# Optimization experiments

Hardware: AMD Instinct MI355X
Metric: run time of the kernel (lower is better)

Reference implementation:

```python
import jax, jax.numpy as jnp
import numpy as np
from jax import lax

EMBED = 512
HEADS = 8
KD = EMBED // HEADS  # key_dim == head_dim (value_factor=1)


def setup_inputs() -> dict:
    key = jax.random.key(0)
    ks = jax.random.split(key, 13)
    b, h, w = 4, 128, 128
    s = 0.02
    return {
        "x": jax.random.normal(ks[0], (b, h, w, EMBED), jnp.float32),
        "mask_h": jax.random.normal(ks[1], (HEADS, h, h), jnp.float32),
        "mask_w": jax.random.normal(ks[2], (HEADS, w, w), jnp.float32),
        "Wq": jax.random.normal(ks[3], (EMBED, EMBED), jnp.float32) * s,
        "bq": jnp.zeros((EMBED,), jnp.float32),
        "Wk": jax.random.normal(ks[4], (EMBED, EMBED), jnp.float32) * s,
        "bk": jnp.zeros((EMBED,), jnp.float32),
        "Wv": jax.random.normal(ks[5], (EMBED, EMBED), jnp.float32) * s,
        "bv": jnp.zeros((EMBED,), jnp.float32),
        "lepe_w": jax.random.normal(ks[6], (5, 5, 1, EMBED), jnp.float32) * s,  # depthwise 5x5, HWIO
        "lepe_b": jnp.zeros((EMBED,), jnp.float32),
        "Wo": jax.random.normal(ks[7], (EMBED, EMBED), jnp.float32) * s,
        "bo": jnp.zeros((EMBED,), jnp.float32),
    }


def reference(x, mask_h, mask_w, Wq, bq, Wk, bk, Wv, bv, lepe_w, lepe_b, Wo, bo):
    b, h, w, _ = x.shape
    scaling = KD ** -0.5
    q = x @ Wq + bq                      # (b,h,w,C)
    k = (x @ Wk + bk) * scaling
    v = x @ Wv + bv

    # depthwise-conv positional term (LePE), 5x5 pad 2, groups=C
    lepe = lax.conv_general_dilated(
        v, lepe_w, window_strides=(1, 1), padding=[(2, 2), (2, 2)],
        dimension_numbers=("NHWC", "HWIO", "NHWC"), feature_group_count=EMBED,
    ) + lepe_b

    qr = q.reshape(b, h, w, HEADS, KD)
    kr = k.reshape(b, h, w, HEADS, KD)
    vr = v.reshape(b, h, w, HEADS, KD)

    # width-axis attention (per row), additive per-head decay mask
    sw = jnp.einsum("bhqnd,bhknd->bhnqk", qr, kr) + mask_w[None, None]  # (b,h,n,w,w)
    Aw = jax.nn.softmax(sw, axis=-1)
    o1 = jnp.einsum("bhnqk,bhknd->bhqnd", Aw, vr)                       # (b,h,w,n,d)

    # height-axis attention (per column) on the width-pass output
    sh = jnp.einsum("bqwnd,bkwnd->bwnqk", qr, kr) + mask_h[None, None]  # (b,w,n,h,h)
    Ah = jax.nn.softmax(sh, axis=-1)
    o2 = jnp.einsum("bwnqk,bkwnd->bqwnd", Ah, o1)                       # (b,h,w,n,d)

    out = o2.reshape(b, h, w, EMBED) + lepe
    return out @ Wo + bo
```

## Files before the change

kernel.cpp:

```cpp
#include <hip/hip_runtime.h>
#include <stdint.h>
#include <stddef.h>

typedef unsigned short u16;
typedef __attribute__((ext_vector_type(8))) short bf16x8;
typedef __attribute__((ext_vector_type(4))) float f32x4;

__device__ __forceinline__ u16 f2bf(float f) {
  union { float f; uint32_t u; } v; v.f = f;
  uint32_t u = v.u;
  return (u16)((u + 0x7FFFu + ((u >> 16) & 1u)) >> 16);
}
__device__ __forceinline__ float bf2f(u16 b) {
  union { uint32_t u; float f; } v; v.u = ((uint32_t)b) << 16;
  return v.f;
}

__device__ __forceinline__ void glds16(const u16* g, u16* l) {
  __builtin_amdgcn_global_load_lds((const __attribute__((address_space(1))) void*)g,
                                   (__attribute__((address_space(3))) void*)l, 16, 0, 0);
}

#define MFMA(a, b, c) __builtin_amdgcn_mfma_f32_16x16x32_bf16((a), (b), (c), 0, 0, 0)


__global__ __launch_bounds__(256) void k_cvt_bf16(const float* __restrict__ in,
                                                  u16* __restrict__ out, int n) {
  int i = (blockIdx.x * 256 + threadIdx.x) * 8;
  if (i >= n) return;
  const float4* p = (const float4*)(in + i);
  float4 a = p[0], b = p[1];
  union { bf16x8 v; u16 s[8]; } o;
  o.s[0] = f2bf(a.x); o.s[1] = f2bf(a.y); o.s[2] = f2bf(a.z); o.s[3] = f2bf(a.w);
  o.s[4] = f2bf(b.x); o.s[5] = f2bf(b.y); o.s[6] = f2bf(b.z); o.s[7] = f2bf(b.w);
  *(bf16x8*)(out + i) = o.v;
}

__global__ __launch_bounds__(256) void k_build_wqkv(
    const float* __restrict__ Wq, const float* __restrict__ bq,
    const float* __restrict__ Wk, const float* __restrict__ bk,
    const float* __restrict__ Wv, const float* __restrict__ bv,
    u16* __restrict__ wT, float* __restrict__ bias) {
  int idx = blockIdx.x * 256 + threadIdx.x;
  int n = idx >> 9, k = idx & 511;
  const float* W; const float* B; int nn; float s = 1.0f;
  if (n < 512)       { W = Wq; B = bq; nn = n; }
  else if (n < 1024) { W = Wk; B = bk; nn = n - 512; s = 0.125f; }
  else               { W = Wv; B = bv; nn = n - 1024; }
  wT[idx] = f2bf(W[(size_t)k * 512 + nn] * s);
  if (k == 0) bias[n] = B[nn] * s;
}

__global__ __launch_bounds__(256) void k_build_wo(const float* __restrict__ Wo,
                                                  u16* __restrict__ wT) {
  int idx = blockIdx.x * 256 + threadIdx.x;
  int n = idx >> 9, k = idx & 511;
  wT[idx] = f2bf(Wo[(size_t)k * 512 + n]);
}


__device__ __forceinline__ void stageH(const u16* __restrict__ src, int ld, size_t grow0,
                                       int kt, int row0, u16* lmat, int t) {
  #pragma unroll
  for (int it = 0; it < 2; ++it) {
    int e = it * 4096 + t * 8;
    int row = row0 + (e >> 6);
    int ch = (e >> 3) & 7;
    int cs = ch ^ (row & 7);
    glds16(src + (grow0 + row) * (size_t)ld + kt * 64 + cs * 8, lmat + row * 64 + ch * 8);
  }
}

__device__ __forceinline__ bf16x8 ldfrag(const u16* lmat, int row, int c) {
  return *(const bf16x8*)(lmat + row * 64 + ((c ^ (row & 7)) << 3));
}

template<bool STAGE, bool VM8>
__device__ __forceinline__ void process_tile(
    const u16* __restrict__ A, int lda, size_t rowA0,
    const u16* __restrict__ BT, int ldb, size_t rowB0,
    u16* LAc, u16* LBc, int nxt,
    int wm, int wn, int fq, int fr, int t,
    f32x4 (&acc)[2][4][2][2])
{
  bf16x8 bA[4][2], bB[2][2][2];
  #pragma unroll
  for (int n = 0; n < 2; ++n)
    #pragma unroll
    for (int kk = 0; kk < 2; ++kk)
      bB[0][n][kk] = ldfrag(LBc, wn * 32 + n * 16 + fr, kk * 4 + fq);
  #pragma unroll
  for (int m = 0; m < 4; ++m)
    #pragma unroll
    for (int kk = 0; kk < 2; ++kk)
      bA[m][kk] = ldfrag(LAc, wm * 64 + m * 16 + fr, kk * 4 + fq);
  __builtin_amdgcn_s_setprio(1);
  #pragma unroll
  for (int m = 0; m < 4; ++m)
    #pragma unroll
    for (int n = 0; n < 2; ++n)
      #pragma unroll
      for (int kk = 0; kk < 2; ++kk)
        acc[0][m][0][n] = MFMA(bA[m][kk], bB[0][n][kk], acc[0][m][0][n]);
  __builtin_amdgcn_s_setprio(0);
  __builtin_amdgcn_s_barrier();
  #pragma unroll
  for (int n = 0; n < 2; ++n)
    #pragma unroll
    for (int kk = 0; kk < 2; ++kk)
      bB[1][n][kk] = ldfrag(LBc, 128 + wn * 32 + n * 16 + fr, kk * 4 + fq);
  if (STAGE) {
    stageH(A, lda, rowA0, nxt, 0, LAc, t);
    stageH(BT, ldb, rowB0, nxt, 0, LBc, t);
  }
  __builtin_amdgcn_s_setprio(1);
  #pragma unroll
  for (int m = 0; m < 4; ++m)
    #pragma unroll
    for (int n = 0; n < 2; ++n)
      #pragma unroll
      for (int kk = 0; kk < 2; ++kk)
        acc[0][m][1][n] = MFMA(bA[m][kk], bB[1][n][kk], acc[0][m][1][n]);
  __builtin_amdgcn_s_setprio(0);
  __builtin_amdgcn_s_barrier();
  #pragma unroll
  for (int m = 0; m < 4; ++m)
    #pragma unroll
    for (int kk = 0; kk < 2; ++kk)
      bA[m][kk] = ldfrag(LAc, 128 + wm * 64 + m * 16 + fr, kk * 4 + fq);
  if (STAGE) stageH(BT, ldb, rowB0, nxt, 128, LBc, t);
  __builtin_amdgcn_s_setprio(1);
  #pragma unroll
  for (int m = 0; m < 4; ++m)
    #pragma unroll
    for (int n = 0; n < 2; ++n)
      #pragma unroll
      for (int kk = 0; kk < 2; ++kk)
        acc[1][m][0][n] = MFMA(bA[m][kk], bB[0][n][kk], acc[1][m][0][n]);
  __builtin_amdgcn_s_setprio(0);
  __builtin_amdgcn_s_barrier();
  if (STAGE) stageH(A, lda, rowA0, nxt, 128, LAc, t);
  __builtin_amdgcn_s_setprio(1);
  #pragma unroll
  for (int m = 0; m < 4; ++m)
    #pragma unroll
    for (int n = 0; n < 2; ++n)
      #pragma unroll
      for (int kk = 0; kk < 2; ++kk)
        acc[1][m][1][n] = MFMA(bA[m][kk], bB[1][n][kk], acc[1][m][1][n]);
  __builtin_amdgcn_s_setprio(0);
  if (VM8) asm volatile("s_waitcnt vmcnt(8)" ::: "memory");
  else     asm volatile("s_waitcnt vmcnt(0)" ::: "memory");
  __builtin_amdgcn_s_barrier();
}

template<bool OUT_F32, int NTN>
__global__ __launch_bounds__(512, 2) void k_gemm256(
    const u16* __restrict__ A, int lda,
    const u16* __restrict__ BT, int ldb,
    const float* __restrict__ bias,
    void* __restrict__ Cp, int ldc)
{
  __shared__ u16 lds[65536];
  u16* LA0 = lds;
  u16* LB0 = lds + 16384;
  u16* LA1 = lds + 32768;
  u16* LB1 = lds + 49152;

  const int t = threadIdx.x, l = t & 63, w = t >> 6;
  const int wm = w >> 2, wn = w & 3;
  const int fq = l >> 4, fr = l & 15;

  const int bid = blockIdx.x;
  const int cpx = gridDim.x >> 3;
  const int swz = (bid & 7) * cpx + (bid >> 3);
  const int tn = swz % NTN, tm = swz / NTN;
  const size_t rowA0 = (size_t)tm * 256;
  const size_t rowB0 = (size_t)tn * 256;

  f32x4 acc[2][4][2][2];
  #pragma unroll
  for (int a = 0; a < 2; ++a)
    #pragma unroll
    for (int m = 0; m < 4; ++m)
      #pragma unroll
      for (int b = 0; b < 2; ++b)
        #pragma unroll
        for (int n = 0; n < 2; ++n) acc[a][m][b][n] = (f32x4){0.f, 0.f, 0.f, 0.f};

  stageH(A,  lda, rowA0, 0, 0,   LA0, t); stageH(A,  lda, rowA0, 0, 128, LA0, t);
  stageH(BT, ldb, rowB0, 0, 0,   LB0, t); stageH(BT, ldb, rowB0, 0, 128, LB0, t);
  stageH(A,  lda, rowA0, 1, 0,   LA1, t); stageH(A,  lda, rowA0, 1, 128, LA1, t);
  stageH(BT, ldb, rowB0, 1, 0,   LB1, t); stageH(BT, ldb, rowB0, 1, 128, LB1, t);
  asm volatile("s_waitcnt vmcnt(8)" ::: "memory");
  __builtin_amdgcn_s_barrier();

  for (int i = 0; i < 3; ++i) {
    process_tile<true, true>(A, lda, rowA0, BT, ldb, rowB0, LA0, LB0, 2 * i + 2,
                             wm, wn, fq, fr, t, acc);
    process_tile<true, true>(A, lda, rowA0, BT, ldb, rowB0, LA1, LB1, 2 * i + 3,
                             wm, wn, fq, fr, t, acc);
  }
  process_tile<false, false>(A, lda, rowA0, BT, ldb, rowB0, LA0, LB0, 0,
                             wm, wn, fq, fr, t, acc);
  process_tile<false, false>(A, lda, rowA0, BT, ldb, rowB0, LA1, LB1, 0,
                             wm, wn, fq, fr, t, acc);

  #pragma unroll
  for (int nh = 0; nh < 2; ++nh)
    #pragma unroll
    for (int n = 0; n < 2; ++n) {
      int col = (int)rowB0 + nh * 128 + wn * 32 + n * 16 + fr;
      float bb = bias[col];
      #pragma unroll
      for (int mh = 0; mh < 2; ++mh)
        #pragma unroll
        for (int m = 0; m < 4; ++m) {
          #pragma unroll
          for (int r = 0; r < 4; ++r) {
            size_t row = rowA0 + mh * 128 + wm * 64 + m * 16 + fq * 4 + r;
            float v = acc[mh][m][nh][n][r] + bb;
            if (OUT_F32) ((float*)Cp)[row * ldc + col] = v;
            else         ((u16*)Cp)[row * ldc + col] = f2bf(v);
          }
        }
    }
}


__global__ __launch_bounds__(256) void k_lepe(
    const u16* __restrict__ qkv, const float* __restrict__ w5,
    const float* __restrict__ lb, u16* __restrict__ outp)
{
  __shared__ u16 wlds[12800];
  #pragma unroll
  for (int j = 0; j < 50; ++j) {
    int idx = j * 256 + threadIdx.x;
    wlds[idx] = f2bf(w5[idx]);
  }
  __syncthreads();

  const int t = threadIdx.x, w = t >> 6, l = t & 63;
  const int c0 = l << 3;
  const int bid = blockIdx.x;
  const int x = (bid & 31) * 4 + w;
  const int y0 = ((bid >> 5) & 15) * 8;
  const int b = bid >> 9;

  float acc[8][8];
  {
    float4 b0 = *(const float4*)(lb + c0);
    float4 b1 = *(const float4*)(lb + c0 + 4);
    #pragma unroll
    for (int tt = 0; tt < 8; ++tt) {
      acc[tt][0] = b0.x; acc[tt][1] = b0.y; acc[tt][2] = b0.z; acc[tt][3] = b0.w;
      acc[tt][4] = b1.x; acc[tt][5] = b1.y; acc[tt][6] = b1.z; acc[tt][7] = b1.w;
    }
  }

  #pragma unroll
  for (int r = 0; r < 12; ++r) {
    int yy = y0 + r - 2;
    if ((unsigned)yy < 128u) {
      #pragma unroll
      for (int dx = 0; dx < 5; ++dx) {
        int xx = x + dx - 2;
        if ((unsigned)xx < 128u) {
          union { bf16x8 v; u16 s[8]; } v8;
          v8.v = *(const bf16x8*)(qkv + (size_t)((b * 128 + yy) * 128 + xx) * 1536
                                  + 1024 + c0);
          float vf[8];
          #pragma unroll
          for (int j = 0; j < 8; ++j) vf[j] = bf2f(v8.s[j]);
          #pragma unroll
          for (int tt = 0; tt < 8; ++tt) {
            int dy = r - tt;
            if (dy >= 0 && dy <= 4) {
              union { bf16x8 v; u16 s[8]; } w8;
              w8.v = *(const bf16x8*)(wlds + (dy * 5 + dx) * 512 + c0);
              #pragma unroll
              for (int j = 0; j < 8; ++j)
                acc[tt][j] += vf[j] * bf2f(w8.s[j]);
            }
          }
        }
      }
    }
  }

  #pragma unroll
  for (int tt = 0; tt < 8; ++tt) {
    size_t tok = (size_t)(b * 128 + y0 + tt) * 128 + x;
    union { bf16x8 v; u16 s[8]; } ov;
    #pragma unroll
    for (int j = 0; j < 8; ++j) ov.s[j] = f2bf(acc[tt][j]);
    *(bf16x8*)(outp + tok * 512 + c0) = ov.v;
  }
}


template<int AXIS>
__global__ __launch_bounds__(256) void k_attn(
    const u16* qkv, const float* __restrict__ mask,
    const u16* __restrict__ lepe, u16* outp)
{
  __shared__ u16 smem[24576];
  u16* q_s = smem;
  u16* k_s = smem + 8192;
  u16* vT  = smem + 16384;
  u16* P   = smem;

  const int t = threadIdx.x, w = t >> 6, l = t & 63;
  const int line = blockIdx.x, head = blockIdx.y, b = blockIdx.z;
  const int coff = head * 64;
  const size_t base0 = (AXIS == 0) ? ((size_t)(b * 128 + line) * 128)
                                   : ((size_t)b * 16384 + line);
  const size_t tstr = (AXIS == 0) ? 1 : 128;

  const int e0 = w * 512 + l * 8;
  #pragma unroll
  for (int it = 0; it < 4; ++it) {
    int ee = it * 2048 + e0;
    int row = ee >> 6;
    int cs = ((ee >> 3) & 7) ^ (row & 7);
    size_t tok = base0 + (size_t)row * tstr;
    glds16(qkv + tok * 1536 +       coff + cs * 8, q_s + it * 2048 + w * 512);
    glds16(qkv + tok * 1536 + 512 + coff + cs * 8, k_s + it * 2048 + w * 512);
  }
  {
    int kl = ((t >> 7) << 4) + (t & 15);
    int chunk = (t >> 4) & 7;
    #pragma unroll
    for (int p = 0; p < 4; ++p) {
      int kidx = p * 32 + kl;
      size_t tok = base0 + (size_t)kidx * tstr;
      union { bf16x8 v; u16 s[8]; } v8;
      v8.v = *(const bf16x8*)(qkv + tok * 1536 + 1024 + coff + chunk * 8);
      #pragma unroll
      for (int j = 0; j < 8; ++j) {
        int d = chunk * 8 + j;
        int byt = d * 256 + ((2 * kidx) ^ (j << 4));
        *(u16*)((char*)vT + byt) = v8.s[j];
      }
    }
  }
  __syncthreads();

  f32x4 acc[2][8];
  #pragma unroll
  for (int m = 0; m < 2; ++m)
    #pragma unroll
    for (int n = 0; n < 8; ++n) acc[m][n] = (f32x4){0.f, 0.f, 0.f, 0.f};

  #pragma unroll
  for (int kk = 0; kk < 2; ++kk) {
    bf16x8 af[2];
    #pragma unroll
    for (int m = 0; m < 2; ++m) {
      int row = w * 32 + m * 16 + (l & 15);
      int c = (kk * 4 + (l >> 4)) ^ (row & 7);
      af[m] = *(const bf16x8*)(q_s + row * 64 + c * 8);
    }
    #pragma unroll
    for (int n = 0; n < 8; ++n) {
      int row = n * 16 + (l & 15);
      int c = (kk * 4 + (l >> 4)) ^ (row & 7);
      bf16x8 bfr = *(const bf16x8*)(k_s + row * 64 + c * 8);
      acc[0][n] = MFMA(af[0], bfr, acc[0][n]);
      acc[1][n] = MFMA(af[1], bfr, acc[1][n]);
    }
  }

  const float* mbase = mask + (size_t)head * 16384;
  #pragma unroll
  for (int m = 0; m < 2; ++m) {
    int q0 = w * 32 + m * 16 + ((l >> 4) << 2);
    #pragma unroll
    for (int n = 0; n < 8; ++n) {
      const float* mp = mbase + (size_t)q0 * 128 + n * 16 + (l & 15);
      #pragma unroll
      for (int r = 0; r < 4; ++r) acc[m][n][r] += mp[(size_t)r * 128];
    }
    #pragma unroll
    for (int r = 0; r < 4; ++r) {
      float mx = acc[m][0][r];
      #pragma unroll
      for (int n = 1; n < 8; ++n) mx = fmaxf(mx, acc[m][n][r]);
      mx = fmaxf(mx, __shfl_xor(mx, 1));
      mx = fmaxf(mx, __shfl_xor(mx, 2));
      mx = fmaxf(mx, __shfl_xor(mx, 4));
      mx = fmaxf(mx, __shfl_xor(mx, 8));
      float sum = 0.f;
      #pragma unroll
      for (int n = 0; n < 8; ++n) {
        float ev = __expf(acc[m][n][r] - mx);
        acc[m][n][r] = ev; sum += ev;
      }
      sum += __shfl_xor(sum, 1);
      sum += __shfl_xor(sum, 2);
      sum += __shfl_xor(sum, 4);
      sum += __shfl_xor(sum, 8);
      float inv = 1.0f / sum;
      #pragma unroll
      for (int n = 0; n < 8; ++n) acc[m][n][r] *= inv;
    }
  }
  __syncthreads();

  #pragma unroll
  for (int m = 0; m < 2; ++m) {
    #pragma unroll
    for (int r = 0; r < 4; ++r) {
      int row = w * 32 + m * 16 + ((l >> 4) << 2) + r;
      int swz = (row & 7) << 4;
      #pragma unroll
      for (int n = 0; n < 8; ++n) {
        int col = n * 16 + (l & 15);
        *(u16*)((char*)P + row * 256 + ((2 * col) ^ swz)) = f2bf(acc[m][n][r]);
      }
    }
  }
  __syncthreads();

  f32x4 o[2][4];
  #pragma unroll
  for (int m = 0; m < 2; ++m)
    #pragma unroll
    for (int n = 0; n < 4; ++n) o[m][n] = (f32x4){0.f, 0.f, 0.f, 0.f};

  #pragma unroll
  for (int kt = 0; kt < 4; ++kt) {
    bf16x8 af[2];
    #pragma unroll
    for (int m = 0; m < 2; ++m) {
      int row = w * 32 + m * 16 + (l & 15);
      af[m] = *(const bf16x8*)((const char*)P + row * 256 +
               ((((kt * 4 + (l >> 4)) << 4)) ^ ((row & 7) << 4)));
    }
    #pragma unroll
    for (int n = 0; n < 4; ++n) {
      int d = n * 16 + (l & 15);
      int byt = d * 256 + (((kt * 32 + (l >> 4) * 8) * 2) ^ ((d & 7) << 4));
      bf16x8 bfr = *(const bf16x8*)((const char*)vT + byt);
      o[0][n] = MFMA(af[0], bfr, o[0][n]);
      o[1][n] = MFMA(af[1], bfr, o[1][n]);
    }
  }

  #pragma unroll
  for (int m = 0; m < 2; ++m) {
    #pragma unroll
    for (int r = 0; r < 4; ++r) {
      int i = w * 32 + m * 16 + ((l >> 4) << 2) + r;
      size_t tok = base0 + (size_t)i * tstr;
      #pragma unroll
      for (int n = 0; n < 4; ++n) {
        int d = n * 16 + (l & 15);
        float v = o[m][n][r];
        if (AXIS == 1) {
          v += bf2f(lepe[tok * 512 + coff + d]);
          outp[tok * 1536 + coff + d] = f2bf(v);
        } else {
          outp[tok * 1536 + 1024 + coff + d] = f2bf(v);
        }
      }
    }
  }
}


extern "C" void kernel_launch(void* const* d_in, const int* in_sizes, int n_in,
                              void* d_out, int out_size, void* d_ws, size_t ws_size,
                              hipStream_t stream) {
  const float* x  = (const float*)d_in[0];
  const float* mh = (const float*)d_in[1];
  const float* mw = (const float*)d_in[2];
  const float* Wq = (const float*)d_in[3];
  const float* bq = (const float*)d_in[4];
  const float* Wk = (const float*)d_in[5];
  const float* bk = (const float*)d_in[6];
  const float* Wv = (const float*)d_in[7];
  const float* bv = (const float*)d_in[8];
  const float* w5 = (const float*)d_in[9];
  const float* lb = (const float*)d_in[10];
  const float* Wo = (const float*)d_in[11];
  const float* bo = (const float*)d_in[12];

  char* ws = (char*)d_ws;
  u16*   qkv   = (u16*)ws;
  u16*   wqkvT = (u16*)(ws + 201326592);
  u16*   woT   = (u16*)(ws + 202899456);
  float* bqkv  = (float*)(ws + 203423744);

  char* od = (char*)d_out;
  u16* xb   = (u16*)od;
  u16* lepe = (u16*)(od + 67108864);

  k_cvt_bf16<<<16384, 256, 0, stream>>>(x, xb, 33554432);
  k_build_wqkv<<<3072, 256, 0, stream>>>(Wq, bq, Wk, bk, Wv, bv, wqkvT, bqkv);
  k_build_wo<<<1024, 256, 0, stream>>>(Wo, woT);

  k_gemm256<false, 6><<<1536, 512, 0, stream>>>(xb, 512, wqkvT, 512, bqkv, qkv, 1536);

  k_lepe<<<2048, 256, 0, stream>>>(qkv, w5, lb, lepe);

  k_attn<0><<<dim3(128, 8, 4), 256, 0, stream>>>(qkv, mw, nullptr, qkv);
  k_attn<1><<<dim3(128, 8, 4), 256, 0, stream>>>(qkv, mh, lepe, qkv);

  k_gemm256<true, 2><<<512, 512, 0, stream>>>(qkv, 1536, woT, 512, bo, d_out, 512);
}
```

Before: 456.7 us.

## Prefetch next K-tile LDS fragments during last MFMA quadrant of GEMM

Restructures the 256x256 GEMM main loop so the A/B register fragments for the next K tile are read from the other LDS buffer during the final MFMA quadrant of the current tile, with fragments carried across calls in persistent register arrays. It adds explicit lgkmcnt(0) waits before barriers, casts LDS reads to address-space-3 pointers, and stops unrolling the outer loop. The aim is to hide LDS read latency behind MFMA work, at the cost of more live registers and extra waits.

Measured after the change: 762.3 us. +66.9%, slower.

```diff
diff --git a/kernel.cpp b/kernel.cpp
--- a/kernel.cpp
+++ b/kernel.cpp
@@ -5,6 +5,8 @@
 typedef unsigned short u16;
 typedef __attribute__((ext_vector_type(8))) short bf16x8;
 typedef __attribute__((ext_vector_type(4))) float f32x4;
+
+typedef __attribute__((address_space(3))) const bf16x8* lds_frag_cptr;
 
 __device__ __forceinline__ u16 f2bf(float f) {
   union { float f; uint32_t u; } v; v.f = f;
@@ -72,43 +74,28 @@
 }
 
 __device__ __forceinline__ bf16x8 ldfrag(const u16* lmat, int row, int c) {
-  return *(const bf16x8*)(lmat + row * 64 + ((c ^ (row & 7)) << 3));
-}
-
-template<bool STAGE, bool VM8>
+  const u16* p = lmat + row * 64 + ((c ^ (row & 7)) << 3);
+  return *(lds_frag_cptr)p;
+}
+
+#define LGKM0_BAR() do { \
+    asm volatile("s_waitcnt lgkmcnt(0)" ::: "memory"); \
+    __builtin_amdgcn_s_barrier(); } while (0)
+
+template<bool STAGE, bool NEXTRD, int VMN>
 __device__ __forceinline__ void process_tile(
     const u16* __restrict__ A, int lda, size_t rowA0,
     const u16* __restrict__ BT, int ldb, size_t rowB0,
-    u16* LAc, u16* LBc, int nxt,
+    u16* LAc, u16* LBc, u16* LAo, u16* LBo, int nxt,
     int wm, int wn, int fq, int fr, int t,
+    bf16x8 (&fA)[2][4][2], bf16x8 (&fB)[2][2][2],
     f32x4 (&acc)[2][4][2][2])
 {
-  bf16x8 bA[4][2], bB[2][2][2];
   #pragma unroll
   for (int n = 0; n < 2; ++n)
     #pragma unroll
     for (int kk = 0; kk < 2; ++kk)
-      bB[0][n][kk] = ldfrag(LBc, wn * 32 + n * 16 + fr, kk * 4 + fq);
-  #pragma unroll
-  for (int m = 0; m < 4; ++m)
-    #pragma unroll
-    for (int kk = 0; kk < 2; ++kk)
-      bA[m][kk] = ldfrag(LAc, wm * 64 + m * 16 + fr, kk * 4 + fq);
-  __builtin_amdgcn_s_setprio(1);
-  #pragma unroll
-  for (int m = 0; m < 4; ++m)
-    #pragma unroll
-    for (int n = 0; n < 2; ++n)
-      #pragma unroll
-      for (int kk = 0; kk < 2; ++kk)
-        acc[0][m][0][n] = MFMA(bA[m][kk], bB[0][n][kk], acc[0][m][0][n]);
-  __builtin_amdgcn_s_setprio(0);
-  __builtin_amdgcn_s_barrier();
-  #pragma unroll
-  for (int n = 0; n < 2; ++n)
-    #pragma unroll
-    for (int kk = 0; kk < 2; ++kk)
-      bB[1][n][kk] = ldfrag(LBc, 128 + wn * 32 + n * 16 + fr, kk * 4 + fq);
+      fB[1][n][kk] = ldfrag(LBc, 128 + wn * 32 + n * 16 + fr, kk * 4 + fq);
   if (STAGE) {
     stageH(A, lda, rowA0, nxt, 0, LAc, t);
     stageH(BT, ldb, rowB0, nxt, 0, LBc, t);
@@ -120,14 +107,14 @@
     for (int n = 0; n < 2; ++n)
       #pragma unroll
       for (int kk = 0; kk < 2; ++kk)
-        acc[0][m][1][n] = MFMA(bA[m][kk], bB[1][n][kk], acc[0][m][1][n]);
+        acc[0][m][0][n] = MFMA(fA[0][m][kk], fB[0][n][kk], acc[0][m][0][n]);
   __builtin_amdgcn_s_setprio(0);
-  __builtin_amdgcn_s_barrier();
+  LGKM0_BAR();
   #pragma unroll
   for (int m = 0; m < 4; ++m)
     #pragma unroll
     for (int kk = 0; kk < 2; ++kk)
-      bA[m][kk] = ldfrag(LAc, 128 + wm * 64 + m * 16 + fr, kk * 4 + fq);
+      fA[1][m][kk] = ldfrag(LAc, 128 + wm * 64 + m * 16 + fr, kk * 4 + fq);
   if (STAGE) stageH(BT, ldb, rowB0, nxt, 128, LBc, t);
   __builtin_amdgcn_s_setprio(1);
   #pragma unroll
@@ -136,9 +123,9 @@
     for (int n = 0; n < 2; ++n)
       #pragma unroll
       for (int kk = 0; kk < 2; ++kk)
-        acc[1][m][0][n] = MFMA(bA[m][kk], bB[0][n][kk], acc[1][m][0][n]);
+        acc[0][m][1][n] = MFMA(fA[0][m][kk], fB[1][n][kk], acc[0][m][1][n]);
   __builtin_amdgcn_s_setprio(0);
-  __builtin_amdgcn_s_barrier();
+  LGKM0_BAR();
   if (STAGE) stageH(A, lda, rowA0, nxt, 128, LAc, t);
   __builtin_amdgcn_s_setprio(1);
   #pragma unroll
@@ -147,11 +134,33 @@
     for (int n = 0; n < 2; ++n)
       #pragma unroll
       for (int kk = 0; kk < 2; ++kk)
-        acc[1][m][1][n] = MFMA(bA[m][kk], bB[1][n][kk], acc[1][m][1][n]);
+        acc[1][m][0][n] = MFMA(fA[1][m][kk], fB[0][n][kk], acc[1][m][0][n]);
   __builtin_amdgcn_s_setprio(0);
-  if (VM8) asm volatile("s_waitcnt vmcnt(8)" ::: "memory");
-  else     asm volatile("s_waitcnt vmcnt(0)" ::: "memory");
-  __builtin_amdgcn_s_barrier();
+  LGKM0_BAR();
+  if (NEXTRD) {
+    if (VMN == 8) asm volatile("s_waitcnt vmcnt(8)" ::: "memory");
+    else          asm volatile("s_waitcnt vmcnt(0)" ::: "memory");
+    #pragma unroll
+    for (int n = 0; n < 2; ++n)
+      #pragma unroll
+      for (int kk = 0; kk < 2; ++kk)
+        fB[0][n][kk] = ldfrag(LBo, wn * 32 + n * 16 + fr, kk * 4 + fq);
+    #pragma unroll
+    for (int m = 0; m < 4; ++m)
+      #pragma unroll
+      for (int kk = 0; kk < 2; ++kk)
+        fA[0][m][kk] = ldfrag(LAo, wm * 64 + m * 16 + fr, kk * 4 + fq);
+  }
+  __builtin_amdgcn_s_setprio(1);
+  #pragma unroll
+  for (int m = 0; m < 4; ++m)
+    #pragma unroll
+    for (int n = 0; n < 2; ++n)
+      #pragma unroll
+      for (int kk = 0; kk < 2; ++kk)
+        acc[1][m][1][n] = MFMA(fA[1][m][kk], fB[1][n][kk], acc[1][m][1][n]);
+  __builtin_amdgcn_s_setprio(0);
+  LGKM0_BAR();
 }
 
 template<bool OUT_F32, int NTN>
@@ -188,23 +197,41 @@
         #pragma unroll
         for (int n = 0; n < 2; ++n) acc[a][m][b][n] = (f32x4){0.f, 0.f, 0.f, 0.f};
 
+  bf16x8 fA[2][4][2], fB[2][2][2];
+
   stageH(A,  lda, rowA0, 0, 0,   LA0, t); stageH(A,  lda, rowA0, 0, 128, LA0, t);
   stageH(BT, ldb, rowB0, 0, 0,   LB0, t); stageH(BT, ldb, rowB0, 0, 128, LB0, t);
   stageH(A,  lda, rowA0, 1, 0,   LA1, t); stageH(A,  lda, rowA0, 1, 128, LA1, t);
   stageH(BT, ldb, rowB0, 1, 0,   LB1, t); stageH(BT, ldb, rowB0, 1, 128, LB1, t);
   asm volatile("s_waitcnt vmcnt(8)" ::: "memory");
   __builtin_amdgcn_s_barrier();
-
+  #pragma unroll
+  for (int n = 0; n < 2; ++n)
+    #pragma unroll
+    for (int kk = 0; kk < 2; ++kk)
+      fB[0][n][kk] = ldfrag(LB0, wn * 32 + n * 16 + fr, kk * 4 + fq);
+  #pragma unroll
+  for (int m = 0; m < 4; ++m)
+    #pragma unroll
+    for (int kk = 0; kk < 2; ++kk)
+      fA[0][m][kk] = ldfrag(LA0, wm * 64 + m * 16 + fr, kk * 4 + fq);
+  LGKM0_BAR();
+
+  #pragma unroll 1
   for (int i = 0; i < 3; ++i) {
-    process_tile<true, true>(A, lda, rowA0, BT, ldb, rowB0, LA0, LB0, 2 * i + 2,
-                             wm, wn, fq, fr, t, acc);
-    process_tile<true, true>(A, lda, rowA0, BT, ldb, rowB0, LA1, LB1, 2 * i + 3,
-                             wm, wn, fq, fr, t, acc);
-  }
-  process_tile<false, false>(A, lda, rowA0, BT, ldb, rowB0, LA0, LB0, 0,
-                             wm, wn, fq, fr, t, acc);
-  process_tile<false, false>(A, lda, rowA0, BT, ldb, rowB0, LA1, LB1, 0,
-                             wm, wn, fq, fr, t, acc);
+    process_tile<true, true, 8>(A, lda, rowA0, BT, ldb, rowB0,
+                                LA0, LB0, LA1, LB1, 2 * i + 2,
+                                wm, wn, fq, fr, t, fA, fB, acc);
+    process_tile<true, true, 8>(A, lda, rowA0, BT, ldb, rowB0,
+                                LA1, LB1, LA0, LB0, 2 * i + 3,
+                                wm, wn, fq, fr, t, fA, fB, acc);
+  }
+  process_tile<false, true, 0>(A, lda, rowA0, BT, ldb, rowB0,
+                               LA0, LB0, LA1, LB1, 0,
+                               wm, wn, fq, fr, t, fA, fB, acc);
+  process_tile<false, false, 0>(A, lda, rowA0, BT, ldb, rowB0,
+                                LA1, LB1, LA0, LB0, 0,
+                                wm, wn, fq, fr, t, fA, fB, acc);
 
   #pragma unroll
   for (int nh = 0; nh < 2; ++nh)
```
